# Kernel optimization log

Measured on AMD Instinct MI355X. Metric: run time of the kernel, lower is better.

The kernel has to match this reference:

```python
import jax, jax.numpy as jnp
import numpy as np

N_NODES = 100000
N_EDGES = 800000
DIM = 64
HEADS = 4
HEAD_DIM = DIM // HEADS  # 16
ALPHA = 0.1
K_ITERS = 8  # fixed-point iterations approximating the implicit/CG solve


def setup_inputs() -> dict:
    key = jax.random.key(0)
    ks = jax.random.split(key, 7)
    x = jax.random.normal(ks[0], (N_NODES, DIM), dtype=jnp.float32)
    edge_index = jax.random.randint(ks[1], (2, N_EDGES), 0, N_NODES, dtype=jnp.int64)
    edge_attr = jax.random.normal(ks[2], (N_EDGES, DIM), dtype=jnp.float32)
    s = 1.0 / np.sqrt(DIM)
    Wq = jax.random.normal(ks[3], (DIM, DIM), dtype=jnp.float32) * s
    Wk = jax.random.normal(ks[4], (DIM, DIM), dtype=jnp.float32) * s
    Wv = jax.random.normal(ks[5], (DIM, DIM), dtype=jnp.float32) * s
    We = jax.random.normal(ks[6], (DIM, DIM), dtype=jnp.float32) * s
    return {"x": x, "edge_index": edge_index, "edge_attr": edge_attr,
            "Wq": Wq, "Wk": Wk, "Wv": Wv, "We": We}


def _mapr(x, edge_index, edge_attr, Wq, Wk, Wv, We):
    N = x.shape[0]
    src, dst = edge_index[0], edge_index[1]
    q = (x @ Wq).reshape(N, HEADS, HEAD_DIM)
    k = (x @ Wk).reshape(N, HEADS, HEAD_DIM)
    v = (x @ Wv).reshape(N, HEADS, HEAD_DIM)
    e = (edge_attr @ We).reshape(-1, HEADS, HEAD_DIM)
    # per-edge multi-head dot attention logits, edge features modulate keys
    logits = jnp.sum(q[dst] * (k[src] + e), axis=-1) / np.sqrt(HEAD_DIM)  # [E,H]
    # segment softmax over incoming edges of each dst node
    m = jax.ops.segment_max(logits, dst, num_segments=N)  # [N,H]
    ex = jnp.exp(logits - m[dst])
    denom = jax.ops.segment_sum(ex, dst, num_segments=N)  # [N,H]
    att = ex / (denom[dst] + 1e-16)  # [E,H]
    # implicit propagation: fixed-point solve of z = alpha*v + (1-alpha) * A_att z
    def step(z, _):
        msg = att[:, :, None] * z[src]                       # [E,H,D]
        agg = jax.ops.segment_sum(msg, dst, num_segments=N)  # [N,H,D]
        return ALPHA * v + (1.0 - ALPHA) * agg, None
    z, _ = jax.lax.scan(step, v, None, length=K_ITERS)
    return z.reshape(N, DIM)


def reference(x, edge_index, edge_attr, Wq, Wk, Wv, We):
    h = _mapr(x, edge_index, edge_attr, Wq, Wk, Wv, We)
    h = jax.nn.relu(h)  # act; dropout is identity in eval mode
    return x + h        # residual
```

## Files before the change

kernel.cpp:

```cpp
#include <hip/hip_runtime.h>
#include <hip/hip_fp16.h>
#include <cstdint>
#include <cstddef>

#define NN 100000
#define NE 800000
#define DIM 64
#define HEADS 4
#define HEAD_DIM 16
#define ALPHA 0.1f
#define K_ITERS 8
#define NBLK 391

typedef short bf16x8 __attribute__((ext_vector_type(8)));
typedef float f32x4 __attribute__((ext_vector_type(4)));
typedef float fvec4 __attribute__((ext_vector_type(4)));

__device__ __forceinline__ unsigned short f2bf(float f) {
    unsigned int x = __float_as_uint(f);
    unsigned int r = (x + 0x7fffu + ((x >> 16) & 1u)) >> 16;
    return (unsigned short)r;
}
__device__ __forceinline__ float bf_lo(unsigned int p) { return __uint_as_float(p << 16); }
__device__ __forceinline__ float bf_hi(unsigned int p) { return __uint_as_float(p & 0xffff0000u); }

__device__ __forceinline__ float2 h2f(unsigned int v) {
    __half2 h = *(__half2*)&v;
    return __half22float2(h);
}
__device__ __forceinline__ unsigned int f2h2(float a, float b) {
    __half2 h = __floats2half2_rn(a, b);
    return *(unsigned int*)&h;
}
__device__ __forceinline__ float dot8h(uint4 a, uint4 b) {
    float2 a0 = h2f(a.x), b0 = h2f(b.x);
    float2 a1 = h2f(a.y), b1 = h2f(b.y);
    float2 a2 = h2f(a.z), b2 = h2f(b.z);
    float2 a3 = h2f(a.w), b3 = h2f(b.w);
    return a0.x * b0.x + a0.y * b0.y + a1.x * b1.x + a1.y * b1.y
         + a2.x * b2.x + a2.y * b2.y + a3.x * b3.x + a3.y * b3.y;
}
__device__ __forceinline__ float dot8bf(fvec4 a0, fvec4 a1, uint4 up) {
    return a0.x * bf_lo(up.x) + a0.y * bf_hi(up.x)
         + a0.z * bf_lo(up.y) + a0.w * bf_hi(up.y)
         + a1.x * bf_lo(up.z) + a1.y * bf_hi(up.z)
         + a1.z * bf_lo(up.w) + a1.w * bf_hi(up.w);
}

#define ACC8(a, V) { float2 t_; \
    t_ = h2f((V).x); m[0] += (a) * t_.x; m[1] += (a) * t_.y; \
    t_ = h2f((V).y); m[2] += (a) * t_.x; m[3] += (a) * t_.y; \
    t_ = h2f((V).z); m[4] += (a) * t_.x; m[5] += (a) * t_.y; \
    t_ = h2f((V).w); m[6] += (a) * t_.x; m[7] += (a) * t_.y; }

__device__ __forceinline__ float rec_att(uint4 r, int head) {
    unsigned int pair = (head & 2) ? r.z : r.y;
    float2 f = h2f(pair);
    return (head & 1) ? f.y : f.x;
}

__global__ __launch_bounds__(256) void qkv_mfma_kernel(
    const float* __restrict__ x,
    const float* __restrict__ Wq, const float* __restrict__ Wk,
    const float* __restrict__ Wv, const float* __restrict__ We,
    __half* __restrict__ qh, __half* __restrict__ kh, __half* __restrict__ vh,
    unsigned short* __restrict__ u)
{
    __shared__ unsigned short sq[64 * 72];
    int tid = threadIdx.x;
    int w = tid >> 6;
    int lane = tid & 63;
    int m16 = lane & 15;
    int quad = lane >> 4;
    int node = blockIdx.x * 64 + w * 16 + m16;
    int nodeC = node < NN ? node : NN - 1;

    bf16x8 afrag[2];
    #pragma unroll
    for (int kk = 0; kk < 2; ++kk) {
        const float* xr = x + (size_t)nodeC * DIM + kk * 32 + quad * 8;
        #pragma unroll
        for (int j = 0; j < 8; ++j) afrag[kk][j] = (short)f2bf(xr[j]);
    }

    const float* Ws[3] = {Wq, Wk, Wv};
    __half* outs[3] = {qh, kh, vh};

    #pragma unroll
    for (int mtx = 0; mtx < 3; ++mtx) {
        const float* W = Ws[mtx];
        #pragma unroll
        for (int n0 = 0; n0 < 64; n0 += 16) {
            int col = n0 + m16;
            f32x4 acc = {0.f, 0.f, 0.f, 0.f};
            #pragma unroll
            for (int kk = 0; kk < 2; ++kk) {
                bf16x8 bfrag;
                #pragma unroll
                for (int j = 0; j < 8; ++j)
                    bfrag[j] = (short)f2bf(W[(kk * 32 + quad * 8 + j) * DIM + col]);
                acc = __builtin_amdgcn_mfma_f32_16x16x32_bf16(afrag[kk], bfrag, acc, 0, 0, 0);
            }
            if (mtx == 0) {
                #pragma unroll
                for (int r = 0; r < 4; ++r) acc[r] *= 0.25f;
            }
            #pragma unroll
            for (int r = 0; r < 4; ++r) {
                int rl = w * 16 + quad * 4 + r;
                int gnode = blockIdx.x * 64 + rl;
                if (mtx == 0) sq[rl * 72 + col] = f2bf(acc[r]);
                if (gnode < NN) outs[mtx][(size_t)gnode * DIM + col] = __float2half(acc[r]);
            }
        }
    }
    __syncthreads();

    #pragma unroll
    for (int h = 0; h < HEADS; ++h) {
        int kk = h >> 1;
        bf16x8 aq;
        const unsigned short* sr = &sq[(w * 16 + m16) * 72 + kk * 32 + quad * 8];
        #pragma unroll
        for (int j = 0; j < 8; ++j) aq[j] = (short)sr[j];
        #pragma unroll
        for (int c0 = 0; c0 < 64; c0 += 16) {
            int c = c0 + m16;
            bf16x8 bfrag;
            #pragma unroll
            for (int j = 0; j < 8; ++j) {
                int k = kk * 32 + quad * 8 + j;
                bfrag[j] = ((k >> 4) == h) ? (short)f2bf(We[c * DIM + k]) : (short)0;
            }
            f32x4 acc = {0.f, 0.f, 0.f, 0.f};
            acc = __builtin_amdgcn_mfma_f32_16x16x32_bf16(aq, bfrag, acc, 0, 0, 0);
            #pragma unroll
            for (int r = 0; r < 4; ++r) {
                int gnode = blockIdx.x * 64 + w * 16 + quad * 4 + r;
                if (gnode < NN) u[(size_t)gnode * 256 + h * 64 + c] = f2bf(acc[r]);
            }
        }
    }
}

__global__ void init_kernel(int* __restrict__ deg) {
    int i = blockIdx.x * 256 + threadIdx.x;
    if (i < NN) deg[i] = 0;
}

__global__ void deg_kernel(const int* __restrict__ ei, int* __restrict__ deg) {
    int e = blockIdx.x * 256 + threadIdx.x;
    if (e >= NE) return;
    atomicAdd(&deg[ei[NE + e]], 1);
}

__global__ void blocksum_kernel(const int* __restrict__ deg, int* __restrict__ bsum) {
    int t = threadIdx.x, b = blockIdx.x;
    int idx = b * 256 + t;
    int v = (idx < NN) ? deg[idx] : 0;
    #pragma unroll
    for (int off = 32; off > 0; off >>= 1) v += __shfl_down(v, off);
    __shared__ int wsum[4];
    if ((t & 63) == 0) wsum[t >> 6] = v;
    __syncthreads();
    if (t == 0) bsum[b] = wsum[0] + wsum[1] + wsum[2] + wsum[3];
}

__global__ void bscan_kernel(const int* __restrict__ bsum, int* __restrict__ boff) {
    __shared__ int s[512];
    int t = threadIdx.x;
    int v = (t < NBLK) ? bsum[t] : 0;
    s[t] = v;
    __syncthreads();
    for (int off = 1; off < 512; off <<= 1) {
        int u = (t >= off) ? s[t - off] : 0;
        __syncthreads();
        s[t] += u;
        __syncthreads();
    }
    if (t < NBLK) boff[t] = s[t] - v;
}

__global__ void rowptr_kernel(const int* __restrict__ deg, const int* __restrict__ boff,
                              int* __restrict__ row_ptr, int* __restrict__ cursor) {
    __shared__ int s[256];
    int t = threadIdx.x, b = blockIdx.x;
    int idx = b * 256 + t;
    int v = (idx < NN) ? deg[idx] : 0;
    s[t] = v;
    __syncthreads();
    for (int off = 1; off < 256; off <<= 1) {
        int u = (t >= off) ? s[t - off] : 0;
        __syncthreads();
        s[t] += u;
        __syncthreads();
    }
    if (idx < NN) {
        int ex = boff[b] + s[t] - v;
        row_ptr[idx] = ex;
        cursor[idx] = ex;
    }
    if (idx == 0) row_ptr[NN] = NE;
}

__global__ void scatter_kernel(const int* __restrict__ ei,
                               int* __restrict__ cursor,
                               int* __restrict__ csr_src,
                               int* __restrict__ csr_e,
                               int* __restrict__ csr_dst) {
    int e = blockIdx.x * 256 + threadIdx.x;
    if (e >= NE) return;
    int src = ei[e], dst = ei[NE + e];
    int pos = atomicAdd(&cursor[dst], 1);
    csr_src[pos] = src;
    csr_e[pos] = e;
    csr_dst[pos] = dst;
}

__global__ __launch_bounds__(256) void logits_csr2_kernel(
    const __half* __restrict__ qh,
    const __half* __restrict__ kh,
    const float* __restrict__ edge_attr,
    const unsigned short* __restrict__ u,
    const int* __restrict__ csr_src,
    const int* __restrict__ csr_e,
    const int* __restrict__ csr_dst,
    uint2* __restrict__ att) {
    int j = blockIdx.x * 256 + threadIdx.x;
    if (j >= NE) return;
    int src = csr_src[j], dst = csr_dst[j], e = csr_e[j];
    const fvec4* attr4 = (const fvec4*)edge_attr + (size_t)e * 16;
    const uint4* urow = (const uint4*)u + (size_t)dst * 32;
    float au0 = 0.f, au1 = 0.f, au2 = 0.f, au3 = 0.f;
    #pragma unroll
    for (int i = 0; i < 8; ++i) {
        fvec4 a0 = __builtin_nontemporal_load(attr4 + 2 * i);
        fvec4 a1 = __builtin_nontemporal_load(attr4 + 2 * i + 1);
        au0 += dot8bf(a0, a1, urow[0 * 8 + i]);
        au1 += dot8bf(a0, a1, urow[1 * 8 + i]);
        au2 += dot8bf(a0, a1, urow[2 * 8 + i]);
        au3 += dot8bf(a0, a1, urow[3 * 8 + i]);
    }
    const uint4* qq = (const uint4*)qh + (size_t)dst * 8;
    const uint4* kk = (const uint4*)kh + (size_t)src * 8;
    float qk0 = dot8h(qq[0], kk[0]) + dot8h(qq[1], kk[1]);
    float qk1 = dot8h(qq[2], kk[2]) + dot8h(qq[3], kk[3]);
    float qk2 = dot8h(qq[4], kk[4]) + dot8h(qq[5], kk[5]);
    float qk3 = dot8h(qq[6], kk[6]) + dot8h(qq[7], kk[7]);
    float e0 = __expf(qk0 + au0);
    float e1 = __expf(qk1 + au1);
    float e2 = __expf(qk2 + au2);
    float e3 = __expf(qk3 + au3);
    uint2 o;
    o.x = f2h2(e0, e1);
    o.y = f2h2(e2, e3);
    att[j] = o;
}

__global__ void recs_fused_kernel(const uint2* __restrict__ att,
                                  const int* __restrict__ csr_src,
                                  const int* __restrict__ row_ptr,
                                  uint4* __restrict__ recs) {
    int n = blockIdx.x * 256 + threadIdx.x;
    if (n >= NN) return;
    int beg = row_ptr[n], end = row_ptr[n + 1];
    float s0 = 1e-16f, s1 = 1e-16f, s2 = 1e-16f, s3 = 1e-16f;
    for (int j = beg; j < end; ++j) {
        uint2 ap = att[j];
        float2 p01 = h2f(ap.x), p23 = h2f(ap.y);
        s0 += p01.x; s1 += p01.y; s2 += p23.x; s3 += p23.y;
    }
    float r0 = 0.9f / s0, r1 = 0.9f / s1, r2 = 0.9f / s2, r3 = 0.9f / s3;
    for (int j = beg; j < end; ++j) {
        uint2 ap = att[j];
        float2 p01 = h2f(ap.x), p23 = h2f(ap.y);
        uint4 rec;
        rec.x = (unsigned int)csr_src[j];
        rec.y = f2h2(p01.x * r0, p01.y * r1);
        rec.z = f2h2(p23.x * r2, p23.y * r3);
        rec.w = 0u;
        recs[j] = rec;
    }
}

__global__ __launch_bounds__(256) void prop_rec_kernel(
    const __half* __restrict__ zin,
    const __half* __restrict__ vh,
    const uint4* __restrict__ recs,
    const int* __restrict__ row_ptr,
    __half* __restrict__ zout) {
    int gid = blockIdx.x * 256 + threadIdx.x;
    int node = gid >> 3;
    if (node >= NN) return;
    int l = gid & 7;
    int head = l >> 1;
    const uint4* z4 = (const uint4*)zin;
    float m[8];
    #pragma unroll
    for (int i = 0; i < 8; ++i) m[i] = 0.f;
    int beg = row_ptr[node], end = row_ptr[node + 1];
    int j = beg;
    for (; j + 8 <= end; j += 8) {
        uint4 r[8], zz[8];
        #pragma unroll
        for (int t = 0; t < 8; ++t) r[t] = recs[j + t];
        #pragma unroll
        for (int t = 0; t < 8; ++t) zz[t] = z4[(size_t)r[t].x * 8 + l];
        #pragma unroll
        for (int t = 0; t < 8; ++t) { float a = rec_att(r[t], head); ACC8(a, zz[t]); }
    }
    for (; j + 4 <= end; j += 4) {
        uint4 r0 = recs[j], r1 = recs[j + 1], r2 = recs[j + 2], r3 = recs[j + 3];
        uint4 z0 = z4[(size_t)r0.x * 8 + l];
        uint4 z1 = z4[(size_t)r1.x * 8 + l];
        uint4 z2 = z4[(size_t)r2.x * 8 + l];
        uint4 z3 = z4[(size_t)r3.x * 8 + l];
        float a0 = rec_att(r0, head), a1 = rec_att(r1, head);
        float a2 = rec_att(r2, head), a3 = rec_att(r3, head);
        ACC8(a0, z0); ACC8(a1, z1); ACC8(a2, z2); ACC8(a3, z3);
    }
    for (; j < end; ++j) {
        uint4 r = recs[j];
        uint4 zl = z4[(size_t)r.x * 8 + l];
        float a = rec_att(r, head);
        ACC8(a, zl);
    }
    uint4 vv = ((const uint4*)vh)[(size_t)node * 8 + l];
    float2 v0 = h2f(vv.x), v1 = h2f(vv.y), v2 = h2f(vv.z), v3 = h2f(vv.w);
    uint4 o;
    o.x = f2h2(ALPHA * v0.x + m[0], ALPHA * v0.y + m[1]);
    o.y = f2h2(ALPHA * v1.x + m[2], ALPHA * v1.y + m[3]);
    o.z = f2h2(ALPHA * v2.x + m[4], ALPHA * v2.y + m[5]);
    o.w = f2h2(ALPHA * v3.x + m[6], ALPHA * v3.y + m[7]);
    ((uint4*)zout)[(size_t)node * 8 + l] = o;
}

__global__ __launch_bounds__(256) void prop_out_rec_kernel(
    const __half* __restrict__ zin,
    const __half* __restrict__ vh,
    const uint4* __restrict__ recs,
    const int* __restrict__ row_ptr,
    const float* __restrict__ x,
    float* __restrict__ out) {
    int gid = blockIdx.x * 256 + threadIdx.x;
    int node = gid >> 3;
    if (node >= NN) return;
    int l = gid & 7;
    int head = l >> 1;
    const uint4* z4 = (const uint4*)zin;
    float m[8];
    #pragma unroll
    for (int i = 0; i < 8; ++i) m[i] = 0.f;
    int beg = row_ptr[node], end = row_ptr[node + 1];
    int j = beg;
    for (; j + 8 <= end; j += 8) {
        uint4 r[8], zz[8];
        #pragma unroll
        for (int t = 0; t < 8; ++t) r[t] = recs[j + t];
        #pragma unroll
        for (int t = 0; t < 8; ++t) zz[t] = z4[(size_t)r[t].x * 8 + l];
        #pragma unroll
        for (int t = 0; t < 8; ++t) { float a = rec_att(r[t], head); ACC8(a, zz[t]); }
    }
    for (; j + 4 <= end; j += 4) {
        uint4 r0 = recs[j], r1 = recs[j + 1], r2 = recs[j + 2], r3 = recs[j + 3];
        uint4 z0 = z4[(size_t)r0.x * 8 + l];
        uint4 z1 = z4[(size_t)r1.x * 8 + l];
        uint4 z2 = z4[(size_t)r2.x * 8 + l];
        uint4 z3 = z4[(size_t)r3.x * 8 + l];
        float a0 = rec_att(r0, head), a1 = rec_att(r1, head);
        float a2 = rec_att(r2, head), a3 = rec_att(r3, head);
        ACC8(a0, z0); ACC8(a1, z1); ACC8(a2, z2); ACC8(a3, z3);
    }
    for (; j < end; ++j) {
        uint4 r = recs[j];
        uint4 zl = z4[(size_t)r.x * 8 + l];
        float a = rec_att(r, head);
        ACC8(a, zl);
    }
    uint4 vv = ((const uint4*)vh)[(size_t)node * 8 + l];
    float2 v0 = h2f(vv.x), v1 = h2f(vv.y), v2 = h2f(vv.z), v3 = h2f(vv.w);
    float zf[8] = { ALPHA * v0.x + m[0], ALPHA * v0.y + m[1],
                    ALPHA * v1.x + m[2], ALPHA * v1.y + m[3],
                    ALPHA * v2.x + m[4], ALPHA * v2.y + m[5],
                    ALPHA * v3.x + m[6], ALPHA * v3.y + m[7] };
    const float4* x4 = (const float4*)x + (size_t)node * 16 + l * 2;
    float4 xa = x4[0], xb = x4[1];
    float4 oa, ob;
    oa.x = xa.x + fmaxf(zf[0], 0.f); oa.y = xa.y + fmaxf(zf[1], 0.f);
    oa.z = xa.z + fmaxf(zf[2], 0.f); oa.w = xa.w + fmaxf(zf[3], 0.f);
    ob.x = xb.x + fmaxf(zf[4], 0.f); ob.y = xb.y + fmaxf(zf[5], 0.f);
    ob.z = xb.z + fmaxf(zf[6], 0.f); ob.w = xb.w + fmaxf(zf[7], 0.f);
    float4* o4 = (float4*)out + (size_t)node * 16 + l * 2;
    o4[0] = oa; o4[1] = ob;
}

extern "C" void kernel_launch(void* const* d_in, const int* in_sizes, int n_in,
                              void* d_out, int out_size, void* d_ws, size_t ws_size,
                              hipStream_t stream) {
    const float* x         = (const float*)d_in[0];
    const int*   ei        = (const int*)d_in[1];
    const float* edge_attr = (const float*)d_in[2];
    const float* Wq        = (const float*)d_in[3];
    const float* Wk        = (const float*)d_in[4];
    const float* Wv        = (const float*)d_in[5];
    const float* We        = (const float*)d_in[6];
    float* out = (float*)d_out;

    __half* qh = (__half*)d_ws;
    __half* kh = qh + (size_t)NN * DIM;
    __half* vh = kh + (size_t)NN * DIM;
    unsigned short* u = (unsigned short*)(vh + (size_t)NN * DIM);
    __half* zha = (__half*)(u + (size_t)NN * 256);
    __half* zhb = zha + (size_t)NN * DIM;
    uint2* att   = (uint2*)(zhb + (size_t)NN * DIM);
    uint4* recs  = (uint4*)(att + (size_t)NE);
    int* deg     = (int*)(recs + (size_t)NE);
    int* bsum    = deg + NN;
    int* boff    = bsum + NBLK;
    int* row_ptr = boff + NBLK;
    int* cursor  = row_ptr + NN + 1;
    int* csr_src = cursor + NN;
    int* csr_e   = csr_src + NE;
    int* csr_dst = csr_e + NE;

    hipLaunchKernelGGL(qkv_mfma_kernel, dim3((NN + 63) / 64), dim3(256), 0, stream,
                       x, Wq, Wk, Wv, We, qh, kh, vh, u);
    hipLaunchKernelGGL(init_kernel, dim3((NN + 255) / 256), dim3(256), 0, stream,
                       deg);
    hipLaunchKernelGGL(deg_kernel, dim3((NE + 255) / 256), dim3(256), 0, stream,
                       ei, deg);
    hipLaunchKernelGGL(blocksum_kernel, dim3(NBLK), dim3(256), 0, stream,
                       deg, bsum);
    hipLaunchKernelGGL(bscan_kernel, dim3(1), dim3(512), 0, stream,
                       bsum, boff);
    hipLaunchKernelGGL(rowptr_kernel, dim3(NBLK), dim3(256), 0, stream,
                       deg, boff, row_ptr, cursor);
    hipLaunchKernelGGL(scatter_kernel, dim3((NE + 255) / 256), dim3(256), 0, stream,
                       ei, cursor, csr_src, csr_e, csr_dst);
    hipLaunchKernelGGL(logits_csr2_kernel, dim3((NE + 255) / 256), dim3(256), 0, stream,
                       qh, kh, edge_attr, u, csr_src, csr_e, csr_dst, att);
    hipLaunchKernelGGL(recs_fused_kernel, dim3((NN + 255) / 256), dim3(256), 0, stream,
                       att, csr_src, row_ptr, recs);

    const __half* zin = vh;
    __half* zout = zha;
    for (int it = 0; it < K_ITERS - 1; ++it) {
        hipLaunchKernelGGL(prop_rec_kernel, dim3((NN * 8 + 255) / 256), dim3(256), 0, stream,
                           zin, vh, recs, row_ptr, zout);
        zin = zout;
        zout = (zout == zha) ? zhb : zha;
    }
    hipLaunchKernelGGL(prop_out_rec_kernel, dim3((NN * 8 + 255) / 256), dim3(256), 0, stream,
                       zin, vh, recs, row_ptr, x, out);
}
```

Baseline: 800.6 us.

## Precompute edge projections via MFMA and degree-sort nodes for balanced propagation

Replaces the per-node q·We^T trick (the u buffer, read per edge) with a direct MFMA projection of edge_attr by We into a half-precision ep buffer, which logits then reads alongside k. It adds a degree-histogram counting sort so nodes are permuted by in-degree, and the CSR and propagation kernels walk nodes in that order, giving wavefronts of similar-degree nodes less divergence. Logits now write recs directly and normalize in place, dropping the separate att buffer. The cost is several extra small launches, an indirection through perm, and zha aliasing the ep region, which is safe only because ep is consumed before propagation starts.

```diff
diff --git a/kernel.cpp b/kernel.cpp
--- a/kernel.cpp
+++ b/kernel.cpp
@@ -15,15 +15,13 @@
 typedef short bf16x8 __attribute__((ext_vector_type(8)));
 typedef float f32x4 __attribute__((ext_vector_type(4)));
 typedef float fvec4 __attribute__((ext_vector_type(4)));
+typedef unsigned int uvec4 __attribute__((ext_vector_type(4)));
 
 __device__ __forceinline__ unsigned short f2bf(float f) {
     unsigned int x = __float_as_uint(f);
     unsigned int r = (x + 0x7fffu + ((x >> 16) & 1u)) >> 16;
     return (unsigned short)r;
 }
-__device__ __forceinline__ float bf_lo(unsigned int p) { return __uint_as_float(p << 16); }
-__device__ __forceinline__ float bf_hi(unsigned int p) { return __uint_as_float(p & 0xffff0000u); }
-
 __device__ __forceinline__ float2 h2f(unsigned int v) {
     __half2 h = *(__half2*)&v;
     return __half22float2(h);
@@ -32,19 +30,15 @@
     __half2 h = __floats2half2_rn(a, b);
     return *(unsigned int*)&h;
 }
-__device__ __forceinline__ float dot8h(uint4 a, uint4 b) {
-    float2 a0 = h2f(a.x), b0 = h2f(b.x);
-    float2 a1 = h2f(a.y), b1 = h2f(b.y);
-    float2 a2 = h2f(a.z), b2 = h2f(b.z);
-    float2 a3 = h2f(a.w), b3 = h2f(b.w);
-    return a0.x * b0.x + a0.y * b0.y + a1.x * b1.x + a1.y * b1.y
-         + a2.x * b2.x + a2.y * b2.y + a3.x * b3.x + a3.y * b3.y;
-}
-__device__ __forceinline__ float dot8bf(fvec4 a0, fvec4 a1, uint4 up) {
-    return a0.x * bf_lo(up.x) + a0.y * bf_hi(up.x)
-         + a0.z * bf_lo(up.y) + a0.w * bf_hi(up.y)
-         + a1.x * bf_lo(up.z) + a1.y * bf_hi(up.z)
-         + a1.z * bf_lo(up.w) + a1.w * bf_hi(up.w);
+__device__ __forceinline__ float dot8s(uvec4 q, uvec4 k, uvec4 e) {
+    float2 qa = h2f(q.x), ka = h2f(k.x), ea = h2f(e.x);
+    float2 qb = h2f(q.y), kb = h2f(k.y), eb = h2f(e.y);
+    float2 qc = h2f(q.z), kc = h2f(k.z), ec = h2f(e.z);
+    float2 qd = h2f(q.w), kd = h2f(k.w), ed = h2f(e.w);
+    return qa.x * (ka.x + ea.x) + qa.y * (ka.y + ea.y)
+         + qb.x * (kb.x + eb.x) + qb.y * (kb.y + eb.y)
+         + qc.x * (kc.x + ec.x) + qc.y * (kc.y + ec.y)
+         + qd.x * (kd.x + ed.x) + qd.y * (kd.y + ed.y);
 }
 
 #define ACC8(a, V) { float2 t_; \
@@ -62,11 +56,9 @@
 __global__ __launch_bounds__(256) void qkv_mfma_kernel(
     const float* __restrict__ x,
     const float* __restrict__ Wq, const float* __restrict__ Wk,
-    const float* __restrict__ Wv, const float* __restrict__ We,
-    __half* __restrict__ qh, __half* __restrict__ kh, __half* __restrict__ vh,
-    unsigned short* __restrict__ u)
+    const float* __restrict__ Wv,
+    __half* __restrict__ qh, __half* __restrict__ kh, __half* __restrict__ vh)
 {
-    __shared__ unsigned short sq[64 * 72];
     int tid = threadIdx.x;
     int w = tid >> 6;
     int lane = tid & 63;
@@ -107,45 +99,60 @@
             }
             #pragma unroll
             for (int r = 0; r < 4; ++r) {
-                int rl = w * 16 + quad * 4 + r;
-                int gnode = blockIdx.x * 64 + rl;
-                if (mtx == 0) sq[rl * 72 + col] = f2bf(acc[r]);
+                int gnode = blockIdx.x * 64 + w * 16 + quad * 4 + r;
                 if (gnode < NN) outs[mtx][(size_t)gnode * DIM + col] = __float2half(acc[r]);
             }
         }
     }
-    __syncthreads();
-
-    #pragma unroll
-    for (int h = 0; h < HEADS; ++h) {
-        int kk = h >> 1;
-        bf16x8 aq;
-        const unsigned short* sr = &sq[(w * 16 + m16) * 72 + kk * 32 + quad * 8];
-        #pragma unroll
-        for (int j = 0; j < 8; ++j) aq[j] = (short)sr[j];
-        #pragma unroll
-        for (int c0 = 0; c0 < 64; c0 += 16) {
-            int c = c0 + m16;
+}
+
+__global__ __launch_bounds__(256) void eproj_mfma_kernel(
+    const float* __restrict__ edge_attr, const float* __restrict__ We,
+    __half* __restrict__ ep)
+{
+    int tid = threadIdx.x;
+    int w = tid >> 6;
+    int lane = tid & 63;
+    int m16 = lane & 15;
+    int quad = lane >> 4;
+    int row = blockIdx.x * 64 + w * 16 + m16;
+
+    bf16x8 afrag[2];
+    #pragma unroll
+    for (int kk = 0; kk < 2; ++kk) {
+        const fvec4* ar = (const fvec4*)(edge_attr + (size_t)row * DIM + kk * 32 + quad * 8);
+        fvec4 a0 = __builtin_nontemporal_load(ar);
+        fvec4 a1 = __builtin_nontemporal_load(ar + 1);
+        afrag[kk][0] = (short)f2bf(a0.x); afrag[kk][1] = (short)f2bf(a0.y);
+        afrag[kk][2] = (short)f2bf(a0.z); afrag[kk][3] = (short)f2bf(a0.w);
+        afrag[kk][4] = (short)f2bf(a1.x); afrag[kk][5] = (short)f2bf(a1.y);
+        afrag[kk][6] = (short)f2bf(a1.z); afrag[kk][7] = (short)f2bf(a1.w);
+    }
+
+    #pragma unroll
+    for (int n0 = 0; n0 < 64; n0 += 16) {
+        int col = n0 + m16;
+        f32x4 acc = {0.f, 0.f, 0.f, 0.f};
+        #pragma unroll
+        for (int kk = 0; kk < 2; ++kk) {
             bf16x8 bfrag;
             #pragma unroll
-            for (int j = 0; j < 8; ++j) {
-                int k = kk * 32 + quad * 8 + j;
-                bfrag[j] = ((k >> 4) == h) ? (short)f2bf(We[c * DIM + k]) : (short)0;
-            }
-            f32x4 acc = {0.f, 0.f, 0.f, 0.f};
-            acc = __builtin_amdgcn_mfma_f32_16x16x32_bf16(aq, bfrag, acc, 0, 0, 0);
-            #pragma unroll
-            for (int r = 0; r < 4; ++r) {
-                int gnode = blockIdx.x * 64 + w * 16 + quad * 4 + r;
-                if (gnode < NN) u[(size_t)gnode * 256 + h * 64 + c] = f2bf(acc[r]);
-            }
+            for (int j = 0; j < 8; ++j)
+                bfrag[j] = (short)f2bf(We[(kk * 32 + quad * 8 + j) * DIM + col]);
+            acc = __builtin_amdgcn_mfma_f32_16x16x32_bf16(afrag[kk], bfrag, acc, 0, 0, 0);
         }
-    }
-}
-
-__global__ void init_kernel(int* __restrict__ deg) {
+        #pragma unroll
+        for (int r = 0; r < 4; ++r) {
+            int grow = blockIdx.x * 64 + w * 16 + quad * 4 + r;
+            ep[(size_t)grow * DIM + col] = __float2half(acc[r]);
+        }
+    }
+}
+
+__global__ void init_kernel(int* __restrict__ deg, int* __restrict__ hist) {
     int i = blockIdx.x * 256 + threadIdx.x;
     if (i < NN) deg[i] = 0;
+    if (i < 64) hist[i] = 0;
 }
 
 __global__ void deg_kernel(const int* __restrict__ ei, int* __restrict__ deg) {
@@ -154,10 +161,35 @@
     atomicAdd(&deg[ei[NE + e]], 1);
 }
 
-__global__ void blocksum_kernel(const int* __restrict__ deg, int* __restrict__ bsum) {
+__global__ void hist_kernel(const int* __restrict__ deg, int* __restrict__ hist) {
+    int n = blockIdx.x * 256 + threadIdx.x;
+    if (n >= NN) return;
+    int d = deg[n]; if (d > 63) d = 63;
+    atomicAdd(&hist[d], 1);
+}
+
+__global__ void binscan_kernel(const int* __restrict__ hist, int* __restrict__ bincur) {
+    if (threadIdx.x == 0) {
+        int acc = 0;
+        for (int d = 0; d < 64; ++d) { bincur[d] = acc; acc += hist[d]; }
+    }
+}
+
+__global__ void permscatter_kernel(const int* __restrict__ deg, int* __restrict__ bincur,
+                                   int* __restrict__ perm, int* __restrict__ rank) {
+    int n = blockIdx.x * 256 + threadIdx.x;
+    if (n >= NN) return;
+    int d = deg[n]; if (d > 63) d = 63;
+    int p = atomicAdd(&bincur[d], 1);
+    perm[p] = n;
+    rank[n] = p;
+}
+
+__global__ void blocksum_kernel(const int* __restrict__ deg, const int* __restrict__ perm,
+                                int* __restrict__ bsum) {
     int t = threadIdx.x, b = blockIdx.x;
     int idx = b * 256 + t;
-    int v = (idx < NN) ? deg[idx] : 0;
+    int v = (idx < NN) ? deg[perm[idx]] : 0;
     #pragma unroll
     for (int off = 32; off > 0; off >>= 1) v += __shfl_down(v, off);
     __shared__ int wsum[4];
@@ -181,12 +213,13 @@
     if (t < NBLK) boff[t] = s[t] - v;
 }
 
-__global__ void rowptr_kernel(const int* __restrict__ deg, const int* __restrict__ boff,
+__global__ void rowptr_kernel(const int* __restrict__ deg, const int* __restrict__ perm,
+                              const int* __restrict__ boff,
                               int* __restrict__ row_ptr, int* __restrict__ cursor) {
     __shared__ int s[256];
     int t = threadIdx.x, b = blockIdx.x;
     int idx = b * 256 + t;
-    int v = (idx < NN) ? deg[idx] : 0;
+    int v = (idx < NN) ? deg[perm[idx]] : 0;
     s[t] = v;
     __syncthreads();
     for (int off = 1; off < 256; off <<= 1) {
@@ -204,6 +237,7 @@
 }
 
 __global__ void scatter_kernel(const int* __restrict__ ei,
+                               const int* __restrict__ rank,
                                int* __restrict__ cursor,
                                int* __restrict__ csr_src,
                                int* __restrict__ csr_e,
@@ -211,75 +245,61 @@
     int e = blockIdx.x * 256 + threadIdx.x;
     if (e >= NE) return;
     int src = ei[e], dst = ei[NE + e];
-    int pos = atomicAdd(&cursor[dst], 1);
+    int pos = atomicAdd(&cursor[rank[dst]], 1);
     csr_src[pos] = src;
     csr_e[pos] = e;
     csr_dst[pos] = dst;
 }
 
-__global__ __launch_bounds__(256) void logits_csr2_kernel(
+__global__ __launch_bounds__(256) void logits_csr3_kernel(
     const __half* __restrict__ qh,
     const __half* __restrict__ kh,
-    const float* __restrict__ edge_attr,
-    const unsigned short* __restrict__ u,
+    const __half* __restrict__ ep,
     const int* __restrict__ csr_src,
     const int* __restrict__ csr_e,
     const int* __restrict__ csr_dst,
-    uint2* __restrict__ att) {
+    uint4* __restrict__ recs) {
     int j = blockIdx.x * 256 + threadIdx.x;
     if (j >= NE) return;
     int src = csr_src[j], dst = csr_dst[j], e = csr_e[j];
-    const fvec4* attr4 = (const fvec4*)edge_attr + (size_t)e * 16;
-    const uint4* urow = (const uint4*)u + (size_t)dst * 32;
-    float au0 = 0.f, au1 = 0.f, au2 = 0.f, au3 = 0.f;
-    #pragma unroll
-    for (int i = 0; i < 8; ++i) {
-        fvec4 a0 = __builtin_nontemporal_load(attr4 + 2 * i);
-        fvec4 a1 = __builtin_nontemporal_load(attr4 + 2 * i + 1);
-        au0 += dot8bf(a0, a1, urow[0 * 8 + i]);
-        au1 += dot8bf(a0, a1, urow[1 * 8 + i]);
-        au2 += dot8bf(a0, a1, urow[2 * 8 + i]);
-        au3 += dot8bf(a0, a1, urow[3 * 8 + i]);
-    }
-    const uint4* qq = (const uint4*)qh + (size_t)dst * 8;
-    const uint4* kk = (const uint4*)kh + (size_t)src * 8;
-    float qk0 = dot8h(qq[0], kk[0]) + dot8h(qq[1], kk[1]);
-    float qk1 = dot8h(qq[2], kk[2]) + dot8h(qq[3], kk[3]);
-    float qk2 = dot8h(qq[4], kk[4]) + dot8h(qq[5], kk[5]);
-    float qk3 = dot8h(qq[6], kk[6]) + dot8h(qq[7], kk[7]);
-    float e0 = __expf(qk0 + au0);
-    float e1 = __expf(qk1 + au1);
-    float e2 = __expf(qk2 + au2);
-    float e3 = __expf(qk3 + au3);
-    uint2 o;
-    o.x = f2h2(e0, e1);
-    o.y = f2h2(e2, e3);
-    att[j] = o;
-}
-
-__global__ void recs_fused_kernel(const uint2* __restrict__ att,
-                                  const int* __restrict__ csr_src,
-                                  const int* __restrict__ row_ptr,
-                                  uint4* __restrict__ recs) {
+    const uvec4* qq = (const uvec4*)qh + (size_t)dst * 8;
+    const uvec4* kk = (const uvec4*)kh + (size_t)src * 8;
+    const uvec4* ee = (const uvec4*)ep + (size_t)e * 8;
+    float lg[4];
+    #pragma unroll
+    for (int h = 0; h < 4; ++h) {
+        uvec4 q0 = qq[2 * h], q1 = qq[2 * h + 1];
+        uvec4 k0 = kk[2 * h], k1 = kk[2 * h + 1];
+        uvec4 e0 = __builtin_nontemporal_load(ee + 2 * h);
+        uvec4 e1 = __builtin_nontemporal_load(ee + 2 * h + 1);
+        lg[h] = dot8s(q0, k0, e0) + dot8s(q1, k1, e1);
+    }
+    uint4 rec;
+    rec.x = (unsigned int)src;
+    rec.y = f2h2(__expf(lg[0]), __expf(lg[1]));
+    rec.z = f2h2(__expf(lg[2]), __expf(lg[3]));
+    rec.w = 0u;
+    recs[j] = rec;
+}
+
+__global__ void recs_fused_kernel(uint4* __restrict__ recs,
+                                  const int* __restrict__ row_ptr) {
     int n = blockIdx.x * 256 + threadIdx.x;
     if (n >= NN) return;
     int beg = row_ptr[n], end = row_ptr[n + 1];
     float s0 = 1e-16f, s1 = 1e-16f, s2 = 1e-16f, s3 = 1e-16f;
     for (int j = beg; j < end; ++j) {
-        uint2 ap = att[j];
-        float2 p01 = h2f(ap.x), p23 = h2f(ap.y);
+        uint4 ap = recs[j];
+        float2 p01 = h2f(ap.y), p23 = h2f(ap.z);
         s0 += p01.x; s1 += p01.y; s2 += p23.x; s3 += p23.y;
     }
     float r0 = 0.9f / s0, r1 = 0.9f / s1, r2 = 0.9f / s2, r3 = 0.9f / s3;
     for (int j = beg; j < end; ++j) {
-        uint2 ap = att[j];
-        float2 p01 = h2f(ap.x), p23 = h2f(ap.y);
-        uint4 rec;
-        rec.x = (unsigned int)csr_src[j];
-        rec.y = f2h2(p01.x * r0, p01.y * r1);
-        rec.z = f2h2(p23.x * r2, p23.y * r3);
-        rec.w = 0u;
-        recs[j] = rec;
+        uint4 ap = recs[j];
+        float2 p01 = h2f(ap.y), p23 = h2f(ap.z);
+        ap.y = f2h2(p01.x * r0, p01.y * r1);
+        ap.z = f2h2(p23.x * r2, p23.y * r3);
+        recs[j] = ap;
     }
 }
 
@@ -288,17 +308,19 @@
     const __half* __restrict__ vh,
     const uint4* __restrict__ recs,
     const int* __restrict__ row_ptr,
+    const int* __restrict__ perm,
     __half* __restrict__ zout) {
     int gid = blockIdx.x * 256 + threadIdx.x;
-    int node = gid >> 3;
-    if (node >= NN) return;
+    int grp = gid >> 3;
+    if (grp >= NN) return;
+    int node = perm[grp];
     int l = gid & 7;
     int head = l >> 1;
     const uint4* z4 = (const uint4*)zin;
     float m[8];
     #pragma unroll
     for (int i = 0; i < 8; ++i) m[i] = 0.f;
-    int beg = row_ptr[node], end = row_ptr[node + 1];
+    int beg = row_ptr[grp], end = row_ptr[grp + 1];
     int j = beg;
     for (; j + 8 <= end; j += 8) {
         uint4 r[8], zz[8];
@@ -340,18 +362,20 @@
     const __half* __restrict__ vh,
     const uint4* __restrict__ recs,
     const int* __restrict__ row_ptr,
+    const int* __restrict__ perm,
     const float* __restrict__ x,
     float* __restrict__ out) {
     int gid = blockIdx.x * 256 + threadIdx.x;
-    int node = gid >> 3;
-    if (node >= NN) return;
+    int grp = gid >> 3;
+    if (grp >= NN) return;
+    int node = perm[grp];
     int l = gid & 7;
     int head = l >> 1;
     const uint4* z4 = (const uint4*)zin;
     float m[8];
     #pragma unroll
     for (int i = 0; i < 8; ++i) m[i] = 0.f;
-    int beg = row_ptr[node], end = row_ptr[node + 1];
+    int beg = row_ptr[grp], end = row_ptr[grp + 1];
     int j = beg;
     for (; j + 8 <= end; j += 8) {
         uint4 r[8], zz[8];
@@ -410,13 +434,16 @@
     __half* qh = (__half*)d_ws;
     __half* kh = qh + (size_t)NN * DIM;
     __half* vh = kh + (size_t)NN * DIM;
-    unsigned short* u = (unsigned short*)(vh + (size_t)NN * DIM);
-    __half* zha = (__half*)(u + (size_t)NN * 256);
+    __half* ep = vh + (size_t)NN * DIM;
+    __half* zha = ep;
     __half* zhb = zha + (size_t)NN * DIM;
-    uint2* att   = (uint2*)(zhb + (size_t)NN * DIM);
-    uint4* recs  = (uint4*)(att + (size_t)NE);
+    uint4* recs  = (uint4*)(ep + (size_t)NE * DIM);
     int* deg     = (int*)(recs + (size_t)NE);
-    int* bsum    = deg + NN;
+    int* perm    = deg + NN;
+    int* rank    = perm + NN;
+    int* hist    = rank + NN;
+    int* bincur  = hist + 64;
+    int* bsum    = bincur + 64;
     int* boff    = bsum + NBLK;
     int* row_ptr = boff + NBLK;
     int* cursor  = row_ptr + NN + 1;
@@ -425,32 +452,40 @@
     int* csr_dst = csr_e + NE;
 
     hipLaunchKernelGGL(qkv_mfma_kernel, dim3((NN + 63) / 64), dim3(256), 0, stream,
-                       x, Wq, Wk, Wv, We, qh, kh, vh, u);
+                       x, Wq, Wk, Wv, qh, kh, vh);
+    hipLaunchKernelGGL(eproj_mfma_kernel, dim3(NE / 64), dim3(256), 0, stream,
+                       edge_attr, We, ep);
     hipLaunchKernelGGL(init_kernel, dim3((NN + 255) / 256), dim3(256), 0, stream,
-                       deg);
+                       deg, hist);
     hipLaunchKernelGGL(deg_kernel, dim3((NE + 255) / 256), dim3(256), 0, stream,
                        ei, deg);
+    hipLaunchKernelGGL(hist_kernel, dim3(NBLK), dim3(256), 0, stream,
+                       deg, hist);
+    hipLaunchKernelGGL(binscan_kernel, dim3(1), dim3(64), 0, stream,
+                       hist, bincur);
+    hipLaunchKernelGGL(permscatter_kernel, dim3(NBLK), dim3(256), 0, stream,
+                       deg, bincur, perm, rank);
     hipLaunchKernelGGL(blocksum_kernel, dim3(NBLK), dim3(256), 0, stream,
-                       deg, bsum);
+                       deg, perm, bsum);
     hipLaunchKernelGGL(bscan_kernel, dim3(1), dim3(512), 0, stream,
                        bsum, boff);
     hipLaunchKernelGGL(rowptr_kernel, dim3(NBLK), dim3(256), 0, stream,
-                       deg, boff, row_ptr, cursor);
+                       deg, perm, boff, row_ptr, cursor);
     hipLaunchKernelGGL(scatter_kernel, dim3((NE + 255) / 256), dim3(256), 0, stream,
-                       ei, cursor, csr_src, csr_e, csr_dst);
-    hipLaunchKernelGGL(logits_csr2_kernel, dim3((NE + 255) / 256), dim3(256), 0, stream,
-                       qh, kh, edge_attr, u, csr_src, csr_e, csr_dst, att);
+                       ei, rank, cursor, csr_src, csr_e, csr_dst);
+    hipLaunchKernelGGL(logits_csr3_kernel, dim3((NE + 255) / 256), dim3(256), 0, stream,
+                       qh, kh, ep, csr_src, csr_e, csr_dst, recs);
     hipLaunchKernelGGL(recs_fused_kernel, dim3((NN + 255) / 256), dim3(256), 0, stream,
-                       att, csr_src, row_ptr, recs);
+                       recs, row_ptr);
 
     const __half* zin = vh;
     __half* zout = zha;
     for (int it = 0; it < K_ITERS - 1; ++it) {
         hipLaunchKernelGGL(prop_rec_kernel, dim3((NN * 8 + 255) / 256), dim3(256), 0, stream,
-                           zin, vh, recs, row_ptr, zout);
+                           zin, vh, recs, row_ptr, perm, zout);
         zin = zout;
         zout = (zout == zha) ? zhb : zha;
     }
     hipLaunchKernelGGL(prop_out_rec_kernel, dim3((NN * 8 + 255) / 256), dim3(256), 0, stream,
-                       zin, vh, recs, row_ptr, x, out);
-}
+                       zin, vh, recs, row_ptr, perm, x, out);
+}
```

New measurement: 1.486 ms. 85.6% more time.
